# Optimization experiments

Measured on AMD Instinct MI355X. Metric: run time of the kernel, lower is better.

## Reference

```python
import jax, jax.numpy as jnp
import numpy as np

NUM_BITS = 8
NUM_STEPS = 2 ** NUM_BITS - 2  # 254, clamp range -127..127


def _roundpass(x):
    # straight-through round: forward=round, backward=identity
    return x + jax.lax.stop_gradient(jnp.round(x) - x)


def _quantize(x, alpha, always_pos=False):
    # Quantizer.quantize with use_ste=True, is_on=True
    alpha = jax.nn.relu(alpha)  # relu(alpha_baseline + alpha_delta)
    stepsize = 2.0 * alpha / NUM_STEPS
    off = alpha if always_pos else 0.0
    scaled = (x - off) / stepsize
    clamped = jnp.clip(_roundpass(scaled), -(NUM_STEPS // 2), NUM_STEPS // 2)
    return clamped * stepsize + off


def setup_inputs() -> dict:
    key = jax.random.key(0)
    k1, k2 = jax.random.split(key)
    x = jax.random.normal(k1, (32, 64, 56, 56), dtype=jnp.float32)
    w = jax.random.normal(k2, (128, 64, 3, 3), dtype=jnp.float32) * 0.05
    alpha_x = jnp.ones((1,), dtype=jnp.float32)
    alpha_w = jnp.ones((1,), dtype=jnp.float32)
    return {"x": x, "w": w, "alpha_x": alpha_x, "alpha_w": alpha_w}


def reference(x, w, alpha_x, alpha_w):
    # quantize activations and weights (8-bit symmetric, STE round)
    qx = _quantize(x, alpha_x[0], always_pos=False)
    qw = _quantize(w, alpha_w[0], always_pos=False)
    # im2col lowering + tiled_mm accumulation over K-tiles is exactly a
    # stride-1 conv with padding (1,1); tile padding in M/N/K contributes
    # only zeros and is sliced off, so plain conv is the faithful math.
    out = jax.lax.conv_general_dilated(
        qx, qw,
        window_strides=(1, 1),
        padding=((1, 1), (1, 1)),
        dimension_numbers=("NCHW", "OIHW", "NCHW"),
    )  # [32, 128, 56, 56]
    return out
```

## Files before the change

kernel.cpp:

```cpp
#include <hip/hip_runtime.h>
#include <hip/hip_bf16.h>

typedef int   v4i __attribute__((ext_vector_type(4)));
typedef float v4f __attribute__((ext_vector_type(4)));

#define HWSZ 3136
#define IMW  56
#define PADW 58
#define PHW  3364
#define CIN  64
#define COUT 128

__device__ __forceinline__ float step_size(float a) {
    a = a > 0.f ? a : 0.f;
    return 2.0f * a / 254.0f;
}

__device__ __forceinline__ int quant1(float x, float s) {
    float v = rintf(x / s);
    v = fminf(127.f, fmaxf(-127.f, v));
    return (int)v;
}

__device__ __forceinline__ unsigned int pack4(int a, int b, int c, int d) {
    return (unsigned int)(a & 255) | ((unsigned int)(b & 255) << 8) |
           ((unsigned int)(c & 255) << 16) | ((unsigned int)(d & 255) << 24);
}

__device__ __forceinline__ void gload_lds16(const signed char* g, signed char* l) {
    __builtin_amdgcn_global_load_lds(
        (const __attribute__((address_space(1))) void*)g,
        (__attribute__((address_space(3))) void*)l, 16, 0, 0);
}

__global__ __launch_bounds__(256) void quant_kernel(const float* __restrict__ x,
                                                    const float* __restrict__ w,
                                                    const float* __restrict__ alpha_x,
                                                    const float* __restrict__ alpha_w,
                                                    signed char* __restrict__ cx,
                                                    signed char* __restrict__ wt) {
    int t = threadIdx.x;
    int b = blockIdx.x;
    if (b >= 392) {
        if (b >= 680) {
            int q = (b - 680) * 256 + t;
            int n = q / 912;
            int r = q % 912;
            int px = r >> 2, seg = r & 3;
            int ph, pw;
            if (px < 58)       { ph = 0;  pw = px; }
            else if (px < 116) { ph = 57; pw = px - 58; }
            else { int k = px - 116; ph = 1 + (k >> 1); pw = (k & 1) * 57; }
            v4i z = {0, 0, 0, 0};
            *(v4i*)(cx + ((size_t)n * PHW + ph * PADW + pw) * 64 + seg * 16) = z;
            return;
        }
        float s = step_size(alpha_w[0]);
        int j = (b - 392) * 256 + t;
        int tap = j / 8192;
        int r   = j % 8192;
        int o   = r >> 6;
        int c   = r & 63;
        float v = w[((size_t)o * 64 + c) * 9 + tap];
        wt[j] = (signed char)quant1(v, s);
        return;
    }

    __shared__ unsigned int tile32[64 * 17];
    float s = step_size(alpha_x[0]);
    int nb  = b / 49;
    int hw0 = (b % 49) * 64;
    int g   = t & 15;
    int cq  = t >> 4;
    int p   = t >> 2;
    int seg = t & 3;
    int hw  = hw0 + p;
    int h   = hw / IMW, wq = hw % IMW;
    signed char* cxp = cx + ((size_t)(h + 1) * PADW + (wq + 1)) * 64 + seg * 16;

#pragma unroll
    for (int i = 0; i < 4; ++i) {
        int n = nb * 4 + i;
        const float* xb = x + ((size_t)n * CIN + cq * 4) * HWSZ + hw0 + g * 4;
        v4f f0 = *(const v4f*)(xb);
        v4f f1 = *(const v4f*)(xb + HWSZ);
        v4f f2 = *(const v4f*)(xb + 2 * HWSZ);
        v4f f3 = *(const v4f*)(xb + 3 * HWSZ);
        if (i) __syncthreads();
#pragma unroll
        for (int j = 0; j < 4; ++j) {
            unsigned int u = pack4(quant1(f0[j], s), quant1(f1[j], s),
                                   quant1(f2[j], s), quant1(f3[j], s));
            tile32[(g * 4 + j) * 17 + cq] = u;
        }
        __syncthreads();
        int base = p * 17 + seg * 4;
        v4i val;
        val[0] = (int)tile32[base + 0];
        val[1] = (int)tile32[base + 1];
        val[2] = (int)tile32[base + 2];
        val[3] = (int)tile32[base + 3];
        *(v4i*)(cxp + (size_t)n * PHW * 64) = val;
    }
}

__global__ __launch_bounds__(128, 1) void conv_kernel(const signed char* __restrict__ cx,
                                                      const signed char* __restrict__ wt,
                                                      const float* __restrict__ ax,
                                                      const float* __restrict__ aw,
                                                      float* __restrict__ out) {
    __shared__ signed char as_[20480];
    float scale = step_size(ax[0]) * step_size(aw[0]);
    int tid  = threadIdx.x;
    int lane = tid & 63;
    int wid  = tid >> 6;
    int row  = lane & 15;
    int kg   = lane >> 4;

    int bid   = blockIdx.x;
    int swz   = (bid & 7) * 196 + (bid >> 3);
    int p0    = swz * 64;
    int n     = p0 / HWSZ;
    int hw0   = p0 % HWSZ;
    int h0    = hw0 / IMW;
    int ustart = h0 - 1; if (ustart > 52) ustart = 52;
    int pstart = ustart + 1;

    const signed char* wsrc = cx + ((size_t)n * PHW + (size_t)pstart * PADW) * 64;
#pragma unroll
    for (int r = 0; r < 10; ++r) {
        int slotbase = r * 128 + wid * 64;
        gload_lds16(wsrc + (size_t)(slotbase + lane) * 16, as_ + slotbase * 16);
    }

    int obase = wid * 64;
    const signed char* wb = wt + (obase + row) * 64 + kg * 16;
    v4i breg[9][4];
#pragma unroll
    for (int tap = 0; tap < 9; ++tap)
#pragma unroll
        for (int ot = 0; ot < 4; ++ot)
            breg[tap][ot] = *(const v4i*)(wb + tap * (COUT * 64) + ot * (16 * 64));

    int lbase[4];
#pragma unroll
    for (int pt = 0; pt < 4; ++pt) {
        int hwp = hw0 + pt * 16 + row;
        int hh  = hwp / IMW, ww = hwp % IMW;
        lbase[pt] = ((hh - ustart) * PADW + (ww + 1)) * 64 + kg * 16;
    }

    asm volatile("s_waitcnt vmcnt(0)" ::: "memory");
    __syncthreads();
#pragma unroll
    for (int tap = 0; tap < 9; ++tap)
#pragma unroll
        for (int ot = 0; ot < 4; ++ot)
            asm volatile("" :: "v"(breg[tap][ot]));

    v4i acc[4][4] = {};

#pragma unroll
    for (int tap = 0; tap < 9; ++tap) {
        int doff = ((tap / 3 - 1) * PADW + (tap % 3 - 1)) * 64;
        v4i a[4];
#pragma unroll
        for (int pt = 0; pt < 4; ++pt)
            a[pt] = *(const v4i*)(as_ + lbase[pt] + doff);
#pragma unroll
        for (int pt = 0; pt < 4; ++pt)
#pragma unroll
            for (int ot = 0; ot < 4; ++ot)
                acc[pt][ot] = __builtin_amdgcn_mfma_i32_16x16x64_i8(a[pt], breg[tap][ot], acc[pt][ot], 0, 0, 0);
    }

#pragma unroll
    for (int pt = 0; pt < 4; ++pt) {
        int hw = hw0 + pt * 16 + kg * 4;
#pragma unroll
        for (int ot = 0; ot < 4; ++ot) {
            int o = obase + ot * 16 + row;
            v4f v;
            v[0] = scale * (float)acc[pt][ot][0];
            v[1] = scale * (float)acc[pt][ot][1];
            v[2] = scale * (float)acc[pt][ot][2];
            v[3] = scale * (float)acc[pt][ot][3];
            *(v4f*)(out + ((size_t)n * COUT + o) * HWSZ + hw) = v;
        }
    }
}

extern "C" void kernel_launch(void* const* d_in, const int* in_sizes, int n_in,
                              void* d_out, int out_size, void* d_ws, size_t ws_size,
                              hipStream_t stream) {
    const float* x  = (const float*)d_in[0];
    const float* w  = (const float*)d_in[1];
    const float* ax = (const float*)d_in[2];
    const float* aw = (const float*)d_in[3];
    float* out = (float*)d_out;

    signed char* cx = (signed char*)d_ws;
    signed char* wt = cx + 6889472;

    quant_kernel<<<794, 256, 0, stream>>>(x, w, ax, aw, cx, wt);
    conv_kernel<<<1568, 128, 0, stream>>>(cx, wt, ax, aw, out);
}
```

Baseline: 33.25 us.

## Process two pixel tiles per conv block with double-buffered LDS staging

```diff
diff --git a/kernel.cpp b/kernel.cpp
--- a/kernel.cpp
+++ b/kernel.cpp
@@ -104,76 +104,53 @@
     }
 }
 
-__global__ __launch_bounds__(128, 1) void conv_kernel(const signed char* __restrict__ cx,
-                                                      const signed char* __restrict__ wt,
-                                                      const float* __restrict__ ax,
-                                                      const float* __restrict__ aw,
-                                                      float* __restrict__ out) {
-    __shared__ signed char as_[20480];
-    float scale = step_size(ax[0]) * step_size(aw[0]);
-    int tid  = threadIdx.x;
-    int lane = tid & 63;
-    int wid  = tid >> 6;
-    int row  = lane & 15;
-    int kg   = lane >> 4;
-
-    int bid   = blockIdx.x;
-    int swz   = (bid & 7) * 196 + (bid >> 3);
-    int p0    = swz * 64;
-    int n     = p0 / HWSZ;
-    int hw0   = p0 % HWSZ;
-    int h0    = hw0 / IMW;
-    int ustart = h0 - 1; if (ustart > 52) ustart = 52;
-    int pstart = ustart + 1;
-
-    const signed char* wsrc = cx + ((size_t)n * PHW + (size_t)pstart * PADW) * 64;
+__device__ __forceinline__ void stage_tile(const signed char* __restrict__ cx,
+                                           int tile, signed char* buf,
+                                           int wid, int lane) {
+    int p0  = tile * 64;
+    int n   = p0 / HWSZ;
+    int hw0 = p0 % HWSZ;
+    int h0  = hw0 / IMW;
+    int us  = h0 - 1; if (us > 52) us = 52;
+    const signed char* src = cx + ((size_t)n * PHW + (size_t)(us + 1) * PADW) * 64;
 #pragma unroll
     for (int r = 0; r < 10; ++r) {
-        int slotbase = r * 128 + wid * 64;
-        gload_lds16(wsrc + (size_t)(slotbase + lane) * 16, as_ + slotbase * 16);
-    }
-
-    int obase = wid * 64;
-    const signed char* wb = wt + (obase + row) * 64 + kg * 16;
-    v4i breg[9][4];
-#pragma unroll
-    for (int tap = 0; tap < 9; ++tap)
-#pragma unroll
-        for (int ot = 0; ot < 4; ++ot)
-            breg[tap][ot] = *(const v4i*)(wb + tap * (COUT * 64) + ot * (16 * 64));
-
+        int slot = r * 128 + wid * 64;
+        gload_lds16(src + (size_t)(slot + lane) * 16, buf + slot * 16);
+    }
+}
+
+__device__ __forceinline__ void compute_store(const signed char* buf,
+                                              const v4i (&breg)[9][4],
+                                              float scale, int tile,
+                                              int obase, int row, int kg,
+                                              float* __restrict__ out) {
+    int p0  = tile * 64;
+    int n   = p0 / HWSZ;
+    int hw0 = p0 % HWSZ;
+    int h0  = hw0 / IMW;
+    int us  = h0 - 1; if (us > 52) us = 52;
     int lbase[4];
 #pragma unroll
     for (int pt = 0; pt < 4; ++pt) {
         int hwp = hw0 + pt * 16 + row;
         int hh  = hwp / IMW, ww = hwp % IMW;
-        lbase[pt] = ((hh - ustart) * PADW + (ww + 1)) * 64 + kg * 16;
-    }
-
-    asm volatile("s_waitcnt vmcnt(0)" ::: "memory");
-    __syncthreads();
-#pragma unroll
-    for (int tap = 0; tap < 9; ++tap)
-#pragma unroll
-        for (int ot = 0; ot < 4; ++ot)
-            asm volatile("" :: "v"(breg[tap][ot]));
-
+        lbase[pt] = ((hh - us) * PADW + (ww + 1)) * 64 + kg * 16;
+    }
     v4i acc[4][4] = {};
-
 #pragma unroll
     for (int tap = 0; tap < 9; ++tap) {
         int doff = ((tap / 3 - 1) * PADW + (tap % 3 - 1)) * 64;
         v4i a[4];
 #pragma unroll
         for (int pt = 0; pt < 4; ++pt)
-            a[pt] = *(const v4i*)(as_ + lbase[pt] + doff);
+            a[pt] = *(const v4i*)(buf + lbase[pt] + doff);
 #pragma unroll
         for (int pt = 0; pt < 4; ++pt)
 #pragma unroll
             for (int ot = 0; ot < 4; ++ot)
                 acc[pt][ot] = __builtin_amdgcn_mfma_i32_16x16x64_i8(a[pt], breg[tap][ot], acc[pt][ot], 0, 0, 0);
     }
-
 #pragma unroll
     for (int pt = 0; pt < 4; ++pt) {
         int hw = hw0 + pt * 16 + kg * 4;
@@ -190,6 +167,51 @@
     }
 }
 
+__global__ __launch_bounds__(128, 1) void conv_kernel(const signed char* __restrict__ cx,
+                                                      const signed char* __restrict__ wt,
+                                                      const float* __restrict__ ax,
+                                                      const float* __restrict__ aw,
+                                                      float* __restrict__ out) {
+    __shared__ signed char as_[2][20480];
+    float scale = step_size(ax[0]) * step_size(aw[0]);
+    int tid  = threadIdx.x;
+    int lane = tid & 63;
+    int wid  = tid >> 6;
+    int row  = lane & 15;
+    int kg   = lane >> 4;
+
+    int bid = blockIdx.x;
+    int swz = (bid & 7) * 98 + (bid >> 3);
+    int t0  = swz * 2;
+    int obase = wid * 64;
+
+    stage_tile(cx, t0, as_[0], wid, lane);
+    const signed char* wb = wt + (obase + row) * 64 + kg * 16;
+    v4i breg[9][4];
+#pragma unroll
+    for (int tap = 0; tap < 9; ++tap)
+#pragma unroll
+        for (int ot = 0; ot < 4; ++ot)
+            breg[tap][ot] = *(const v4i*)(wb + tap * (COUT * 64) + ot * (16 * 64));
+
+    asm volatile("s_waitcnt vmcnt(0)" ::: "memory");
+    __syncthreads();
+#pragma unroll
+    for (int tap = 0; tap < 9; ++tap)
+#pragma unroll
+        for (int ot = 0; ot < 4; ++ot)
+            asm volatile("" :: "v"(breg[tap][ot]));
+
+    stage_tile(cx, t0 + 1, as_[1], wid, lane);
+    compute_store(as_[0], breg, scale, t0, obase, row, kg, out);
+
+    asm volatile("s_waitcnt vmcnt(16)" ::: "memory");
+    __builtin_amdgcn_s_barrier();
+    __builtin_amdgcn_sched_barrier(0);
+
+    compute_store(as_[1], breg, scale, t0 + 1, obase, row, kg, out);
+}
+
 extern "C" void kernel_launch(void* const* d_in, const int* in_sizes, int n_in,
                               void* d_out, int out_size, void* d_ws, size_t ws_size,
                               hipStream_t stream) {
@@ -203,5 +225,5 @@
     signed char* wt = cx + 6889472;
 
     quant_kernel<<<794, 256, 0, stream>>>(x, w, ax, aw, cx, wt);
-    conv_kernel<<<1568, 128, 0, stream>>>(cx, wt, ax, aw, out);
-}
+    conv_kernel<<<784, 128, 0, stream>>>(cx, wt, ax, aw, out);
+}
```

Result: slower. 35.13 us (+5.6%).
